# Kernel tuning notes

Hardware: AMD Instinct MI355X
Metric: run time of the kernel (lower is better)

## Reference

```python
import jax, jax.numpy as jnp
import numpy as np

N_TOKEN = 267735
CUTOFFS = [20000, 40000, 200000, 267735]
ENDS = [0] + CUTOFFS
CLUSTER_DIMS = [1024, 256, 64, 16]   # d_embed // div_val**i
CLUSTER_SIZES = [20000, 20000, 160000, 67735]
D_PROJ = 1024
T, B = 256, 4
N_CLUSTERS = 3


def setup_inputs() -> dict:
    key = jax.random.key(0)
    ks = jax.random.split(key, 16)
    inp = {}
    inp["hidden"] = jax.random.normal(ks[0], (T, B, D_PROJ), jnp.float32)
    inp["target"] = jax.random.randint(ks[1], (T, B), 0, N_TOKEN)
    for i in range(4):
        inp[f"W{i}"] = jax.random.normal(ks[2 + 3 * i], (CLUSTER_SIZES[i], CLUSTER_DIMS[i]), jnp.float32) * 0.02
        inp[f"b{i}"] = jnp.zeros((CLUSTER_SIZES[i],), jnp.float32)
        inp[f"P{i}"] = jax.random.normal(ks[3 + 3 * i], (CLUSTER_DIMS[i], D_PROJ), jnp.float32) * 0.02
    inp["cluster_weight"] = jax.random.normal(ks[14], (N_CLUSTERS, 1024), jnp.float32) * 0.02
    inp["cluster_bias"] = jnp.zeros((N_CLUSTERS,), jnp.float32)
    return inp


def _logit(x, W, b, P):
    # x: [T,B,d_proj], P: [e,d_proj], W: [n,e] -> [T,B,n]
    y = jnp.einsum('ibd,ed->ibe', x, P)
    return jnp.einsum('ibe,ne->ibn', y, W) + b


def _gather(logprob, tgt):
    # pick logprob[t, b, tgt[t,b]]
    return jnp.take_along_axis(logprob, tgt[..., None], axis=-1)[..., 0]


def reference(hidden, target, W0, b0, P0, W1, b1, P1, W2, b2, P2, W3, b3, P3,
              cluster_weight, cluster_bias):
    Ws = [W0, W1, W2, W3]
    bs = [b0, b1, b2, b3]
    Ps = [P0, P1, P2, P3]
    loss = jnp.zeros(target.shape, jnp.float32)
    head_logprob = None
    for i in range(4):
        l_idx, r_idx = ENDS[i], ENDS[i + 1]
        mask = (target >= l_idx) & (target < r_idx)
        cur_t = jnp.maximum(jnp.minimum(target, r_idx - 1) - l_idx, 0)
        if i == 0:
            Wh = jnp.concatenate([W0, cluster_weight], axis=0)
            bh = jnp.concatenate([b0, cluster_bias], axis=0)
            head_logprob = jax.nn.log_softmax(_logit(hidden, Wh, bh, P0), axis=-1)
            cur_loss = _gather(head_logprob, cur_t)
        else:
            tail_logprob = jax.nn.log_softmax(_logit(hidden, Ws[i], bs[i], Ps[i]), axis=-1)
            logprob_i = head_logprob[..., CUTOFFS[0] + i - 1, None] + tail_logprob
            cur_loss = _gather(logprob_i, cur_t)
        loss = jnp.where(mask, cur_loss, loss)
    return jnp.mean(-loss)
```

## Files before the change

kernel.cpp:

```cpp
#include <hip/hip_runtime.h>
#include <math.h>

typedef short short8 __attribute__((ext_vector_type(8)));
typedef float f32x4 __attribute__((ext_vector_type(4)));
typedef unsigned long long u64;

#define LOG2E 1.4426950408889634f

__device__ __forceinline__ unsigned short f2bf_rne(float f) {
    unsigned u = __float_as_uint(f);
    unsigned r = (u + 0x7fff + ((u >> 16) & 1)) >> 16;
    return (unsigned short)r;
}
__device__ __forceinline__ float bf2f(unsigned short h) {
    return __uint_as_float(((unsigned)h) << 16);
}
__device__ __forceinline__ void load_lds16(const void* g, void* l) {
    __builtin_amdgcn_global_load_lds((const __attribute__((address_space(1))) void*)g,
                                     (__attribute__((address_space(3))) void*)l,
                                     16, 0, 0);
}
__device__ __forceinline__ u64 pack8_fp8(const float* v, float s) {
    int lo = 0, hi = 0;
    lo = __builtin_amdgcn_cvt_pk_fp8_f32(v[0] * s, v[1] * s, lo, false);
    lo = __builtin_amdgcn_cvt_pk_fp8_f32(v[2] * s, v[3] * s, lo, true);
    hi = __builtin_amdgcn_cvt_pk_fp8_f32(v[4] * s, v[5] * s, hi, false);
    hi = __builtin_amdgcn_cvt_pk_fp8_f32(v[6] * s, v[7] * s, hi, true);
    return (u64)(unsigned)lo | ((u64)(unsigned)hi << 32);
}

__global__ void cvt_h(const float* __restrict__ in, unsigned short* __restrict__ out)
{
    const int i = blockIdx.x * 256 + threadIdx.x;
    const float4 v = *(const float4*)(in + (size_t)i * 4);
    ushort4 h;
    h.x = f2bf_rne(v.x); h.y = f2bf_rne(v.y);
    h.z = f2bf_rne(v.z); h.w = f2bf_rne(v.w);
    *(ushort4*)(out + (size_t)i * 4) = h;
}

struct ProjDesc {
    const float* B;
    unsigned short* Cbf;
    unsigned char* Cf8;
    int ldc; int nreal; int N; int Kpad; int gy_begin;
};

__global__ __launch_bounds__(256) void prepproj(
    const unsigned short* __restrict__ A,
    ProjDesc p0, ProjDesc p1, ProjDesc p2, ProjDesc p3,
    const float* __restrict__ W0, const float* __restrict__ cw,
    const float* __restrict__ W1, const float* __restrict__ W2,
    const float* __restrict__ W3,
    const float* __restrict__ b0, const float* __restrict__ cb,
    const float* __restrict__ b1, const float* __restrict__ b2,
    const float* __restrict__ b3,
    unsigned char* __restrict__ Wb0, unsigned char* __restrict__ Wb1,
    unsigned char* __restrict__ Wb2, unsigned char* __restrict__ Wb3,
    float* __restrict__ bp)
{
    __shared__ char smem[34816];

    const int tid = threadIdx.x;
    const int bx = blockIdx.x;

    if (bx >= 96) {
        const unsigned E0 = 1286144u;
        const unsigned E1 = 1613824u;
        const unsigned E2 = 2260992u;
        const unsigned E3 = 2539520u;
        const unsigned E4 = 2607520u;
        const unsigned stride = (gridDim.x - 96) * 256u;
        for (unsigned u = (bx - 96) * 256u + tid; u < E4; u += stride) {
            if (u < E3) {
                const float* src = nullptr;
                unsigned char* dstm; unsigned tile, kg2, r, tstride;
                if (u < E0) {
                    tile = u >> 13; const unsigned rem = u & 8191u;
                    kg2 = rem >> 7; r = rem & 127u;
                    const unsigned row = tile * 128u + r;
                    if (row < 20000u)      src = W0 + (size_t)row * 1024 + kg2 * 16;
                    else if (row < 20003u) src = cw + (size_t)(row - 20000u) * 1024 + kg2 * 16;
                    dstm = Wb0; tstride = 131072u;
                } else if (u < E1) {
                    const unsigned j = u - E0;
                    tile = j >> 11; const unsigned rem = j & 2047u;
                    kg2 = rem >> 7; r = rem & 127u;
                    const unsigned row = tile * 128u + r;
                    if (row < 20000u) src = W1 + (size_t)row * 256 + kg2 * 16;
                    dstm = Wb1; tstride = 32768u;
                } else if (u < E2) {
                    const unsigned j = u - E1;
                    tile = j >> 9; kg2 = (j >> 7) & 3u; r = j & 127u;
                    const unsigned row = tile * 128u + r;
                    if (row < 160000u) src = W2 + (size_t)row * 64 + kg2 * 16;
                    dstm = Wb2; tstride = 8192u;
                } else {
                    const unsigned j = u - E2;
                    tile = j >> 9; kg2 = (j >> 7) & 3u; r = j & 127u;
                    const unsigned row = tile * 128u + r;
                    if (kg2 == 0 && row < 67735u) src = W3 + (size_t)row * 16;
                    dstm = Wb3; tstride = 8192u;
                }
                float f[16];
                if (src) {
#pragma unroll
                    for (int q = 0; q < 4; ++q) {
                        const float4 v = *(const float4*)(src + q * 4);
                        f[q * 4 + 0] = v.x; f[q * 4 + 1] = v.y;
                        f[q * 4 + 2] = v.z; f[q * 4 + 3] = v.w;
                    }
                } else {
#pragma unroll
                    for (int q = 0; q < 16; ++q) f[q] = 0.f;
                }
                u64* dst = (u64*)(dstm + (size_t)tile * tstride);
                dst[(2 * kg2) * 128 + r]     = pack8_fp8(f,     16.0f);
                dst[(2 * kg2 + 1) * 128 + r] = pack8_fp8(f + 8, 16.0f);
            } else {
                const unsigned idx0 = (u - E3) * 4u;
                float e[4];
#pragma unroll
                for (int j = 0; j < 4; ++j) {
                    const unsigned idx = idx0 + j;
                    float v;
                    if (idx < 20096u) {
                        v = (idx < 20000u) ? b0[idx] * LOG2E
                          : (idx < 20003u) ? cb[idx - 20000u] * LOG2E : -1e30f;
                    } else if (idx < 40576u) {
                        const unsigned i1 = idx - 20096u;
                        v = (i1 < 20000u) ? b1[i1] * LOG2E : -1e30f;
                    } else if (idx < 202368u) {
                        const unsigned i2 = idx - 40576u;
                        v = (i2 < 160000u) ? b2[i2] * LOG2E : -1e30f;
                    } else {
                        const unsigned i3 = idx - 202368u;
                        v = (i3 < 67735u) ? b3[i3] * LOG2E : -1e30f;
                    }
                    e[j] = v;
                }
                *(float4*)(bp + idx0) = make_float4(e[0], e[1], e[2], e[3]);
            }
        }
        return;
    }

    unsigned short* As = (unsigned short*)smem;
    unsigned short* Bs = (unsigned short*)(smem + 16384);

    const int mt = bx & 7;
    const int py = bx >> 3;
    ProjDesc p = (py >= p3.gy_begin) ? p3 : (py >= p2.gy_begin) ? p2
               : (py >= p1.gy_begin) ? p1 : p0;

    const int w = tid >> 6;
    const int l = tid & 63;
    const int m0 = mt * 128;
    const int n0 = (py - p.gy_begin) * 128;
    const int wm = (w >> 1) * 64;
    const int wn = (w & 1) * 64;
    const int lane16 = l & 15;
    const int quad = l >> 4;

    const unsigned short* aptr[4];
    int ag_base[4];
#pragma unroll
    for (int i = 0; i < 4; ++i) {
        const int g = w * 256 + i * 64 + l;
        aptr[i] = A + (size_t)(m0 + (g & 127)) * 1024 + (g >> 7) * 8;
        ag_base[i] = (w * 256 + i * 64) * 8;
    }

    const int bn = tid >> 1;
    const int bhalf = tid & 1;
    int brow = n0 + bn;
    if (brow > p.N - 1) brow = p.N - 1;
    const float* brow_ptr = p.B + (size_t)brow * 1024;

    f32x4 acc[4][4] = {};

    for (int k0 = 0; k0 < 1024; k0 += 64) {
        __syncthreads();
#pragma unroll
        for (int i = 0; i < 4; ++i)
            load_lds16(aptr[i] + k0, (void*)&As[ag_base[i]]);
#pragma unroll
        for (int j = 0; j < 8; ++j) {
            const int kq = bhalf * 8 + j;
            const float4 v = *(const float4*)(brow_ptr + k0 + kq * 4);
            const unsigned px = __builtin_amdgcn_perm(__float_as_uint(v.y), __float_as_uint(v.x), 0x07060302);
            const unsigned pyv = __builtin_amdgcn_perm(__float_as_uint(v.w), __float_as_uint(v.z), 0x07060302);
            const int gran = (kq >> 1) * 128 + bn;
            *(uint2*)&Bs[gran * 8 + (kq & 1) * 4] = make_uint2(px, pyv);
        }
        __syncthreads();

#pragma unroll
        for (int kk = 0; kk < 2; ++kk) {
            const int kgb = kk * 4 + quad;
            short8 af[4], bfr[4];
#pragma unroll
            for (int mi = 0; mi < 4; ++mi)
                af[mi] = *(const short8*)&As[(kgb * 128 + wm + mi * 16 + lane16) * 8];
#pragma unroll
            for (int ni = 0; ni < 4; ++ni)
                bfr[ni] = *(const short8*)&Bs[(kgb * 128 + wn + ni * 16 + lane16) * 8];
#pragma unroll
            for (int mi = 0; mi < 4; ++mi)
#pragma unroll
                for (int ni = 0; ni < 4; ++ni)
                    acc[mi][ni] = __builtin_amdgcn_mfma_f32_16x16x32_bf16(
                        af[mi], bfr[ni], acc[mi][ni], 0, 0, 0);
        }
    }

#pragma unroll
    for (int mi = 0; mi < 4; ++mi)
#pragma unroll
        for (int ni = 0; ni < 4; ++ni) {
            const int n = n0 + wn + ni * 16 + lane16;
            if (n < p.ldc) {
#pragma unroll
                for (int r = 0; r < 4; ++r) {
                    const int m = m0 + wm + mi * 16 + quad * 4 + r;
                    const float v = (n < p.nreal) ? acc[mi][ni][r] : 0.f;
                    p.Cbf[(size_t)m * p.ldc + n] = f2bf_rne(v);
                }
            }
        }

    float* bounce = (float*)smem;
    u64* Yout = (u64*)p.Cf8 + (size_t)mt * 16 * p.Kpad;
    for (int c = 0; c < 2; ++c) {
        const int colbase = n0 + c * 64;
        if (colbase >= p.Kpad) break;
        __syncthreads();
        if ((w & 1) == c) {
#pragma unroll
            for (int mi = 0; mi < 4; ++mi)
#pragma unroll
                for (int ni = 0; ni < 4; ++ni) {
                    const int ncol = ni * 16 + lane16;
                    const bool real = (colbase + ncol) < p.nreal;
#pragma unroll
                    for (int r = 0; r < 4; ++r) {
                        const int m = wm + mi * 16 + quad * 4 + r;
                        bounce[m * 66 + ncol] = real ? acc[mi][ni][r] : 0.f;
                    }
                }
        }
        __syncthreads();
#pragma unroll
        for (int i = 0; i < 4; ++i) {
            const int g = i * 256 + tid;
            const int kgl = g >> 7;
            const int m = g & 127;
            float v[8];
#pragma unroll
            for (int j = 0; j < 8; ++j) v[j] = bounce[m * 66 + kgl * 8 + j];
            Yout[((colbase >> 3) + kgl) * 128 + m] = pack8_fp8(v, 4.0f);
        }
    }
}

struct ExpDesc {
    const unsigned char* A;
    const unsigned char* W;
    const float* bias;
    float* part;
    int Kpad; int ksl; int kmask; int gy_begin; int slab;
};

__global__ __launch_bounds__(256) void exp_gemm(ExpDesc d0, ExpDesc d1, ExpDesc d2, ExpDesc d3)
{
    __shared__ u64 As[2][1024];
    __shared__ u64 Bs[2][1024];
    __shared__ float buf[128][2];

    const int gy = blockIdx.y;
    ExpDesc d = (gy >= d3.gy_begin) ? d3 : (gy >= d2.gy_begin) ? d2
              : (gy >= d1.gy_begin) ? d1 : d0;

    const int tid = threadIdx.x;
    const int w = tid >> 6;
    const int l = tid & 63;
    const int mt = blockIdx.x;
    const int wm = (w >> 1) * 64;
    const int wn = (w & 1) * 64;
    const int lane16 = l & 15;
    const int quad = l >> 4;

    const int tiles_begin = (gy - d.gy_begin) * d.slab;
    const int T = d.slab << d.ksl;
    const int kmask = d.kmask;
    const int ksl = d.ksl;

    const size_t tstride = (size_t)128 * d.Kpad;
    const unsigned char* Abase = d.A + (size_t)mt * tstride;
    const unsigned char* Bbase = d.W + (size_t)tiles_begin * tstride;

    const int so0 = tid * 16;
    const int so1 = 4096 + tid * 16;

    load_lds16(Abase + so0, (char*)As[0] + so0);
    load_lds16(Abase + so1, (char*)As[0] + so1);
    load_lds16(Bbase + so0, (char*)Bs[0] + so0);
    load_lds16(Bbase + so1, (char*)Bs[0] + so1);

    float biasc[4], biasn[4];
#pragma unroll
    for (int ni = 0; ni < 4; ++ni)
        biasc[ni] = d.bias[tiles_begin * 128 + wn + ni * 16 + lane16];
#pragma unroll
    for (int ni = 0; ni < 4; ++ni) biasn[ni] = 0.f;

    f32x4 acc[4][4] = {};
    float rowsum[4][4] = {};
    const float c1 = LOG2E / 64.0f;

    for (int it = 0; it < T; ++it) {
        const int slot = it & 1;
        __syncthreads();

        if (it + 1 < T) {
            const int ns = slot ^ 1;
            const int kc = (it + 1) & kmask;
            if (kmask) {
                const unsigned char* ac = Abase + kc * 8192;
                load_lds16(ac + so0, (char*)As[ns] + so0);
                load_lds16(ac + so1, (char*)As[ns] + so1);
            }
            const unsigned char* bc = Bbase + (size_t)((it + 1) >> ksl) * tstride + kc * 8192;
            load_lds16(bc + so0, (char*)Bs[ns] + so0);
            load_lds16(bc + so1, (char*)Bs[ns] + so1);
            if (kc == 0) {
#pragma unroll
                for (int ni = 0; ni < 4; ++ni)
                    biasn[ni] = d.bias[(tiles_begin + ((it + 1) >> ksl)) * 128 + wn + ni * 16 + lane16];
            }
        }

        const u64* Ar = As[kmask ? slot : 0];
        const u64* Br = Bs[slot];
#pragma unroll
        for (int ks = 0; ks < 2; ++ks) {
            u64 af[4], bfr[4];
#pragma unroll
            for (int mi = 0; mi < 4; ++mi)
                af[mi] = Ar[(ks * 4 + quad) * 128 + wm + mi * 16 + lane16];
#pragma unroll
            for (int ni = 0; ni < 4; ++ni)
                bfr[ni] = Br[(ks * 4 + quad) * 128 + wn + ni * 16 + lane16];
#pragma unroll
            for (int mi = 0; mi < 4; ++mi)
#pragma unroll
                for (int ni = 0; ni < 4; ++ni)
                    acc[mi][ni] = __builtin_amdgcn_mfma_f32_16x16x32_fp8_fp8(
                        (long)af[mi], (long)bfr[ni], acc[mi][ni], 0, 0, 0);
        }

        if ((it & kmask) == kmask) {
#pragma unroll
            for (int mi = 0; mi < 4; ++mi)
#pragma unroll
                for (int r = 0; r < 4; ++r) {
                    float s = exp2f(fmaf(acc[mi][0][r], c1, biasc[0]))
                            + exp2f(fmaf(acc[mi][1][r], c1, biasc[1]))
                            + exp2f(fmaf(acc[mi][2][r], c1, biasc[2]))
                            + exp2f(fmaf(acc[mi][3][r], c1, biasc[3]));
                    rowsum[mi][r] += s;
                }
#pragma unroll
            for (int mi = 0; mi < 4; ++mi)
#pragma unroll
                for (int ni = 0; ni < 4; ++ni)
                    acc[mi][ni] = (f32x4){0.f, 0.f, 0.f, 0.f};
#pragma unroll
            for (int ni = 0; ni < 4; ++ni) biasc[ni] = biasn[ni];
        }
    }

#pragma unroll
    for (int off = 1; off < 16; off <<= 1)
#pragma unroll
        for (int mi = 0; mi < 4; ++mi)
#pragma unroll
            for (int r = 0; r < 4; ++r)
                rowsum[mi][r] += __shfl_xor(rowsum[mi][r], off, 64);

    __syncthreads();
    if (lane16 == 0) {
#pragma unroll
        for (int mi = 0; mi < 4; ++mi)
#pragma unroll
            for (int r = 0; r < 4; ++r)
                buf[wm + mi * 16 + quad * 4 + r][wn >> 6] = rowsum[mi][r];
    }
    __syncthreads();
    if (tid < 128)
        d.part[(size_t)(gy - d.gy_begin) * 1024 + mt * 128 + tid] = buf[tid][0] + buf[tid][1];
}

__global__ void redext(const float* __restrict__ p0, const float* __restrict__ p1,
                       const float* __restrict__ p2, const float* __restrict__ p3,
                       float* __restrict__ S,
                       const unsigned short* __restrict__ Y0, const unsigned short* __restrict__ Y1,
                       const unsigned short* __restrict__ Y2, const unsigned short* __restrict__ Y3,
                       const int* __restrict__ target,
                       const float* __restrict__ W0, const float* __restrict__ b0,
                       const float* __restrict__ W1, const float* __restrict__ b1,
                       const float* __restrict__ W2, const float* __restrict__ b2,
                       const float* __restrict__ W3, const float* __restrict__ b3,
                       const float* __restrict__ cw, const float* __restrict__ cb,
                       float* __restrict__ headlogit, float* __restrict__ taillogit)
{
    if (blockIdx.x < 16) {
        const int idx = blockIdx.x * 256 + threadIdx.x;
        const int c = idx >> 10, m = idx & 1023;
        const float* p = (c == 0) ? p0 : (c == 1) ? p1 : (c == 2) ? p2 : p3;
        const int G = (c == 0) ? 157 : (c == 1) ? 40 : (c == 2) ? 79 : 34;
        float s = 0.f;
        for (int y = 0; y < G; ++y) s += p[(size_t)y * 1024 + m];
        S[idx] = s;
        return;
    }
    const int token = (blockIdx.x - 16) * 4 + (threadIdx.x >> 6);
    const int lane = threadIdx.x & 63;
    const int tgt = target[token];
    const int ci = (tgt < 20000) ? 0 : (tgt < 40000) ? 1 : (tgt < 200000) ? 2 : 3;

    {
        const int h = (ci == 0) ? tgt : (20000 + ci - 1);
        const float* row;
        float bb;
        if (h < 20000) { row = W0 + (size_t)h * 1024; bb = b0[h]; }
        else           { row = cw + (size_t)(h - 20000) * 1024; bb = cb[h - 20000]; }
        const unsigned short* y = Y0 + (size_t)token * 1024;
        float s = 0.f;
        for (int k = lane; k < 1024; k += 64) s += bf2f(y[k]) * row[k];
#pragma unroll
        for (int off = 1; off < 64; off <<= 1) s += __shfl_xor(s, off, 64);
        if (lane == 0) headlogit[token] = s + bb;
    }

    float tl = 0.f;
    if (ci > 0) {
        const unsigned short* Y; const float* W; const float* b; int K, ldy, lidx;
        if (ci == 1)      { Y = Y1; W = W1; b = b1; K = 256; ldy = 256; lidx = 20000; }
        else if (ci == 2) { Y = Y2; W = W2; b = b2; K = 64;  ldy = 64;  lidx = 40000; }
        else              { Y = Y3; W = W3; b = b3; K = 16;  ldy = 64;  lidx = 200000; }
        const int r = tgt - lidx;
        const unsigned short* y = Y + (size_t)token * ldy;
        const float* row = W + (size_t)r * K;
        float s = 0.f;
        for (int k = lane; k < K; k += 64) s += bf2f(y[k]) * row[k];
#pragma unroll
        for (int off = 1; off < 64; off <<= 1) s += __shfl_xor(s, off, 64);
        tl = s + b[r];
    }
    if (lane == 0) taillogit[token] = tl;
}

__global__ void finalize_kernel(const float* __restrict__ S,
                                const int* __restrict__ target,
                                const float* __restrict__ headlogit,
                                const float* __restrict__ taillogit,
                                float* __restrict__ out)
{
    __shared__ float red[256];
    const int tid = threadIdx.x;
    float acc = 0.f;
    for (int token = tid; token < 1024; token += 256) {
        const int tgt = target[token];
        const int ci = (tgt < 20000) ? 0 : (tgt < 40000) ? 1 : (tgt < 200000) ? 2 : 3;
        float lp = headlogit[token] - logf(S[token]);
        if (ci > 0)
            lp += taillogit[token] - logf(S[ci * 1024 + token]);
        acc -= lp;
    }
    red[tid] = acc;
    __syncthreads();
    for (int s = 128; s > 0; s >>= 1) {
        if (tid < s) red[tid] += red[tid + s];
        __syncthreads();
    }
    if (tid == 0) out[0] = red[0] * (1.0f / 1024.0f);
}

extern "C" void kernel_launch(void* const* d_in, const int* in_sizes, int n_in,
                              void* d_out, int out_size, void* d_ws, size_t ws_size,
                              hipStream_t stream)
{
    const float* hidden = (const float*)d_in[0];
    const int*   target = (const int*)d_in[1];
    const float* W0 = (const float*)d_in[2];  const float* b0 = (const float*)d_in[3];  const float* P0 = (const float*)d_in[4];
    const float* W1 = (const float*)d_in[5];  const float* b1 = (const float*)d_in[6];  const float* P1 = (const float*)d_in[7];
    const float* W2 = (const float*)d_in[8];  const float* b2 = (const float*)d_in[9];  const float* P2 = (const float*)d_in[10];
    const float* W3 = (const float*)d_in[11]; const float* b3 = (const float*)d_in[12]; const float* P3 = (const float*)d_in[13];
    const float* cw = (const float*)d_in[14]; const float* cb = (const float*)d_in[15];
    float* out = (float*)d_out;

    unsigned char* ws = (unsigned char*)d_ws;
    unsigned short* h_bf = (unsigned short*)ws;
    unsigned short* Y0bf = (unsigned short*)(ws + 2097152);
    unsigned short* Y1bf = (unsigned short*)(ws + 4194304);
    unsigned short* Y2bf = (unsigned short*)(ws + 4718592);
    unsigned short* Y3bf = (unsigned short*)(ws + 4849664);
    unsigned char* Y0f8 = ws + 4980736;
    unsigned char* Y1f8 = ws + 6029312;
    unsigned char* Y2f8 = ws + 6291456;
    unsigned char* Y3f8 = ws + 6356992;
    unsigned char* Wb0 = ws + 6422528;
    unsigned char* Wb1 = ws + 27000832;
    unsigned char* Wb2 = ws + 32243712;
    unsigned char* Wb3 = ws + 42598400;
    float* bp = (float*)(ws + 47054848);

    float* part0 = (float*)ws;
    float* part1 = part0 + (size_t)157 * 1024;
    float* part2 = part1 + (size_t)40 * 1024;
    float* part3 = part2 + (size_t)79 * 1024;
    float* S = part3 + (size_t)34 * 1024;
    float* headlogit = S + 4096;
    float* taillogit = headlogit + 1024;

    cvt_h<<<1024, 256, 0, stream>>>(hidden, h_bf);

    ProjDesc pr0 = { P0, Y0bf, Y0f8, 1024, 1024, 1024, 1024, 0 };
    ProjDesc pr1 = { P1, Y1bf, Y1f8, 256,  256,  256,  256,  8 };
    ProjDesc pr2 = { P2, Y2bf, Y2f8, 64,   64,   64,   64,   10 };
    ProjDesc pr3 = { P3, Y3bf, Y3f8, 64,   16,   16,   64,   11 };
    prepproj<<<2048, 256, 0, stream>>>(h_bf, pr0, pr1, pr2, pr3,
                                       W0, cw, W1, W2, W3,
                                       b0, cb, b1, b2, b3,
                                       Wb0, Wb1, Wb2, Wb3, bp);

    ExpDesc d0 = { Y0f8, Wb0, bp,          part0, 1024, 4, 15, 0,   1 };
    ExpDesc d1 = { Y1f8, Wb1, bp + 20096,  part1, 256,  2, 3,  157, 4 };
    ExpDesc d2 = { Y2f8, Wb2, bp + 40576,  part2, 64,   0, 0,  197, 16 };
    ExpDesc d3 = { Y3f8, Wb3, bp + 202368, part3, 64,   0, 0,  276, 16 };
    exp_gemm<<<dim3(8, 310), 256, 0, stream>>>(d0, d1, d2, d3);

    redext<<<272, 256, 0, stream>>>(part0, part1, part2, part3, S,
                                    Y0bf, Y1bf, Y2bf, Y3bf, target,
                                    W0, b0, W1, b1, W2, b2, W3, b3,
                                    cw, cb, headlogit, taillogit);

    finalize_kernel<<<1, 256, 0, stream>>>(S, target, headlogit, taillogit, out);
}
```

Before: 438.6 us.

## Widen exp GEMM tile to 256 columns, fuse hidden bf16 cast into projection

The exp_gemm kernel now processes two 128-column weight tiles per block (a 128x256 output tile with 8 N-fragments per wave). This halves the grid rows and reuses each A fragment across twice as many MFMAs, at the cost of more accumulator registers and LDS. The separate cvt_h launch is removed, and the projection GEMM now reads fp32 hidden directly and converts it to bf16 while staging into LDS. The weight-repack path uses one block per fixed chunk instead of a grid-stride loop, and the slab counts, bias padding and workspace offsets are retuned to match.

```diff
diff --git a/kernel.cpp b/kernel.cpp
--- a/kernel.cpp
+++ b/kernel.cpp
@@ -29,16 +29,6 @@
     return (u64)(unsigned)lo | ((u64)(unsigned)hi << 32);
 }
 
-__global__ void cvt_h(const float* __restrict__ in, unsigned short* __restrict__ out)
-{
-    const int i = blockIdx.x * 256 + threadIdx.x;
-    const float4 v = *(const float4*)(in + (size_t)i * 4);
-    ushort4 h;
-    h.x = f2bf_rne(v.x); h.y = f2bf_rne(v.y);
-    h.z = f2bf_rne(v.z); h.w = f2bf_rne(v.w);
-    *(ushort4*)(out + (size_t)i * 4) = h;
-}
-
 struct ProjDesc {
     const float* B;
     unsigned short* Cbf;
@@ -47,7 +37,7 @@
 };
 
 __global__ __launch_bounds__(256) void prepproj(
-    const unsigned short* __restrict__ A,
+    const float* __restrict__ hidden,
     ProjDesc p0, ProjDesc p1, ProjDesc p2, ProjDesc p3,
     const float* __restrict__ W0, const float* __restrict__ cw,
     const float* __restrict__ W1, const float* __restrict__ W2,
@@ -65,79 +55,72 @@
     const int bx = blockIdx.x;
 
     if (bx >= 96) {
-        const unsigned E0 = 1286144u;
-        const unsigned E1 = 1613824u;
-        const unsigned E2 = 2260992u;
-        const unsigned E3 = 2539520u;
-        const unsigned E4 = 2607520u;
-        const unsigned stride = (gridDim.x - 96) * 256u;
-        for (unsigned u = (bx - 96) * 256u + tid; u < E4; u += stride) {
-            if (u < E3) {
-                const float* src = nullptr;
-                unsigned char* dstm; unsigned tile, kg2, r, tstride;
-                if (u < E0) {
-                    tile = u >> 13; const unsigned rem = u & 8191u;
-                    kg2 = rem >> 7; r = rem & 127u;
-                    const unsigned row = tile * 128u + r;
-                    if (row < 20000u)      src = W0 + (size_t)row * 1024 + kg2 * 16;
-                    else if (row < 20003u) src = cw + (size_t)(row - 20000u) * 1024 + kg2 * 16;
-                    dstm = Wb0; tstride = 131072u;
-                } else if (u < E1) {
-                    const unsigned j = u - E0;
-                    tile = j >> 11; const unsigned rem = j & 2047u;
-                    kg2 = rem >> 7; r = rem & 127u;
-                    const unsigned row = tile * 128u + r;
-                    if (row < 20000u) src = W1 + (size_t)row * 256 + kg2 * 16;
-                    dstm = Wb1; tstride = 32768u;
-                } else if (u < E2) {
-                    const unsigned j = u - E1;
-                    tile = j >> 9; kg2 = (j >> 7) & 3u; r = j & 127u;
-                    const unsigned row = tile * 128u + r;
-                    if (row < 160000u) src = W2 + (size_t)row * 64 + kg2 * 16;
-                    dstm = Wb2; tstride = 8192u;
-                } else {
-                    const unsigned j = u - E2;
-                    tile = j >> 9; kg2 = (j >> 7) & 3u; r = j & 127u;
-                    const unsigned row = tile * 128u + r;
-                    if (kg2 == 0 && row < 67735u) src = W3 + (size_t)row * 16;
-                    dstm = Wb3; tstride = 8192u;
+        const int v = bx - 96;
+        if (v < 9896) {
+            const float* src = nullptr;
+            u64* dst;
+            unsigned kseg, r;
+            if (v < 5056) {
+                const unsigned u = v * 256u + tid;
+                const unsigned tile = u >> 13; kseg = (u >> 7) & 63u; r = u & 127u;
+                const unsigned row = tile * 128u + r;
+                if (row < 20000u)      src = W0 + (size_t)row * 1024 + kseg * 16;
+                else if (row < 20003u) src = cw + (size_t)(row - 20000u) * 1024 + kseg * 16;
+                dst = (u64*)Wb0 + (size_t)tile * 16384;
+            } else if (v < 6336) {
+                const unsigned u = (v - 5056) * 256u + tid;
+                const unsigned tile = u >> 11; kseg = (u >> 7) & 15u; r = u & 127u;
+                const unsigned row = tile * 128u + r;
+                if (row < 20000u) src = W1 + (size_t)row * 256 + kseg * 16;
+                dst = (u64*)Wb1 + (size_t)tile * 4096;
+            } else if (v < 8836) {
+                const unsigned u = (v - 6336) * 256u + tid;
+                const unsigned tile = u >> 9; kseg = (u >> 7) & 3u; r = u & 127u;
+                src = W2 + (size_t)(tile * 128u + r) * 64 + kseg * 16;
+                dst = (u64*)Wb2 + (size_t)tile * 1024;
+            } else {
+                const unsigned u = (v - 8836) * 256u + tid;
+                const unsigned tile = u >> 9; kseg = (u >> 7) & 3u; r = u & 127u;
+                const unsigned row = tile * 128u + r;
+                if (kseg == 0 && row < 67735u) src = W3 + (size_t)row * 16;
+                dst = (u64*)Wb3 + (size_t)tile * 1024;
+            }
+            float f[16];
+            if (src) {
+#pragma unroll
+                for (int q = 0; q < 4; ++q) {
+                    const float4 x = *(const float4*)(src + q * 4);
+                    f[q * 4 + 0] = x.x; f[q * 4 + 1] = x.y;
+                    f[q * 4 + 2] = x.z; f[q * 4 + 3] = x.w;
                 }
-                float f[16];
-                if (src) {
-#pragma unroll
-                    for (int q = 0; q < 4; ++q) {
-                        const float4 v = *(const float4*)(src + q * 4);
-                        f[q * 4 + 0] = v.x; f[q * 4 + 1] = v.y;
-                        f[q * 4 + 2] = v.z; f[q * 4 + 3] = v.w;
-                    }
-                } else {
-#pragma unroll
-                    for (int q = 0; q < 16; ++q) f[q] = 0.f;
-                }
-                u64* dst = (u64*)(dstm + (size_t)tile * tstride);
-                dst[(2 * kg2) * 128 + r]     = pack8_fp8(f,     16.0f);
-                dst[(2 * kg2 + 1) * 128 + r] = pack8_fp8(f + 8, 16.0f);
             } else {
-                const unsigned idx0 = (u - E3) * 4u;
+#pragma unroll
+                for (int q = 0; q < 16; ++q) f[q] = 0.f;
+            }
+            dst[(2 * kseg) * 128 + r]     = pack8_fp8(f,     16.0f);
+            dst[(2 * kseg + 1) * 128 + r] = pack8_fp8(f + 8, 16.0f);
+        } else {
+            const unsigned u = (v - 9896) * 256u + tid;
+            if (u < 67136u) {
+                const unsigned idx0 = u * 4u;
                 float e[4];
 #pragma unroll
                 for (int j = 0; j < 4; ++j) {
                     const unsigned idx = idx0 + j;
-                    float v;
-                    if (idx < 20096u) {
-                        v = (idx < 20000u) ? b0[idx] * LOG2E
+                    float x;
+                    if (idx < 20224u) {
+                        x = (idx < 20000u) ? b0[idx] * LOG2E
                           : (idx < 20003u) ? cb[idx - 20000u] * LOG2E : -1e30f;
-                    } else if (idx < 40576u) {
-                        const unsigned i1 = idx - 20096u;
-                        v = (i1 < 20000u) ? b1[i1] * LOG2E : -1e30f;
-                    } else if (idx < 202368u) {
-                        const unsigned i2 = idx - 40576u;
-                        v = (i2 < 160000u) ? b2[i2] * LOG2E : -1e30f;
+                    } else if (idx < 40704u) {
+                        const unsigned i1 = idx - 20224u;
+                        x = (i1 < 20000u) ? b1[i1] * LOG2E : -1e30f;
+                    } else if (idx < 200704u) {
+                        x = b2[idx - 40704u] * LOG2E;
                     } else {
-                        const unsigned i3 = idx - 202368u;
-                        v = (i3 < 67735u) ? b3[i3] * LOG2E : -1e30f;
+                        const unsigned i3 = idx - 200704u;
+                        x = (i3 < 67735u) ? b3[i3] * LOG2E : -1e30f;
                     }
-                    e[j] = v;
+                    e[j] = x;
                 }
                 *(float4*)(bp + idx0) = make_float4(e[0], e[1], e[2], e[3]);
             }
@@ -162,18 +145,10 @@
     const int lane16 = l & 15;
     const int quad = l >> 4;
 
-    const unsigned short* aptr[4];
-    int ag_base[4];
-#pragma unroll
-    for (int i = 0; i < 4; ++i) {
-        const int g = w * 256 + i * 64 + l;
-        aptr[i] = A + (size_t)(m0 + (g & 127)) * 1024 + (g >> 7) * 8;
-        ag_base[i] = (w * 256 + i * 64) * 8;
-    }
-
-    const int bn = tid >> 1;
-    const int bhalf = tid & 1;
-    int brow = n0 + bn;
+    const int sn = tid >> 1;
+    const int shalf = tid & 1;
+    const float* arow_ptr = hidden + (size_t)(m0 + sn) * 1024;
+    int brow = n0 + sn;
     if (brow > p.N - 1) brow = p.N - 1;
     const float* brow_ptr = p.B + (size_t)brow * 1024;
 
@@ -182,16 +157,21 @@
     for (int k0 = 0; k0 < 1024; k0 += 64) {
         __syncthreads();
 #pragma unroll
-        for (int i = 0; i < 4; ++i)
-            load_lds16(aptr[i] + k0, (void*)&As[ag_base[i]]);
-#pragma unroll
         for (int j = 0; j < 8; ++j) {
-            const int kq = bhalf * 8 + j;
-            const float4 v = *(const float4*)(brow_ptr + k0 + kq * 4);
-            const unsigned px = __builtin_amdgcn_perm(__float_as_uint(v.y), __float_as_uint(v.x), 0x07060302);
-            const unsigned pyv = __builtin_amdgcn_perm(__float_as_uint(v.w), __float_as_uint(v.z), 0x07060302);
-            const int gran = (kq >> 1) * 128 + bn;
-            *(uint2*)&Bs[gran * 8 + (kq & 1) * 4] = make_uint2(px, pyv);
+            const int kq = shalf * 8 + j;
+            const int gran = (kq >> 1) * 128 + sn;
+            {
+                const float4 x = *(const float4*)(arow_ptr + k0 + kq * 4);
+                const unsigned px = __builtin_amdgcn_perm(__float_as_uint(x.y), __float_as_uint(x.x), 0x07060302);
+                const unsigned py2 = __builtin_amdgcn_perm(__float_as_uint(x.w), __float_as_uint(x.z), 0x07060302);
+                *(uint2*)&As[gran * 8 + (kq & 1) * 4] = make_uint2(px, py2);
+            }
+            {
+                const float4 x = *(const float4*)(brow_ptr + k0 + kq * 4);
+                const unsigned px = __builtin_amdgcn_perm(__float_as_uint(x.y), __float_as_uint(x.x), 0x07060302);
+                const unsigned py2 = __builtin_amdgcn_perm(__float_as_uint(x.w), __float_as_uint(x.z), 0x07060302);
+                *(uint2*)&Bs[gran * 8 + (kq & 1) * 4] = make_uint2(px, py2);
+            }
         }
         __syncthreads();
 
@@ -223,8 +203,8 @@
 #pragma unroll
                 for (int r = 0; r < 4; ++r) {
                     const int m = m0 + wm + mi * 16 + quad * 4 + r;
-                    const float v = (n < p.nreal) ? acc[mi][ni][r] : 0.f;
-                    p.Cbf[(size_t)m * p.ldc + n] = f2bf_rne(v);
+                    const float x = (n < p.nreal) ? acc[mi][ni][r] : 0.f;
+                    p.Cbf[(size_t)m * p.ldc + n] = f2bf_rne(x);
                 }
             }
         }
@@ -255,10 +235,10 @@
             const int g = i * 256 + tid;
             const int kgl = g >> 7;
             const int m = g & 127;
-            float v[8];
-#pragma unroll
-            for (int j = 0; j < 8; ++j) v[j] = bounce[m * 66 + kgl * 8 + j];
-            Yout[((colbase >> 3) + kgl) * 128 + m] = pack8_fp8(v, 4.0f);
+            float x[8];
+#pragma unroll
+            for (int j = 0; j < 8; ++j) x[j] = bounce[m * 66 + kgl * 8 + j];
+            Yout[((colbase >> 3) + kgl) * 128 + m] = pack8_fp8(x, 4.0f);
         }
     }
 }
@@ -274,7 +254,7 @@
 __global__ __launch_bounds__(256) void exp_gemm(ExpDesc d0, ExpDesc d1, ExpDesc d2, ExpDesc d3)
 {
     __shared__ u64 As[2][1024];
-    __shared__ u64 Bs[2][1024];
+    __shared__ u64 Bs[2][2048];
     __shared__ float buf[128][2];
 
     const int gy = blockIdx.y;
@@ -290,31 +270,38 @@
     const int lane16 = l & 15;
     const int quad = l >> 4;
 
-    const int tiles_begin = (gy - d.gy_begin) * d.slab;
+    const int dt_begin = (gy - d.gy_begin) * d.slab;
     const int T = d.slab << d.ksl;
     const int kmask = d.kmask;
     const int ksl = d.ksl;
 
     const size_t tstride = (size_t)128 * d.Kpad;
     const unsigned char* Abase = d.A + (size_t)mt * tstride;
-    const unsigned char* Bbase = d.W + (size_t)tiles_begin * tstride;
+    const unsigned char* Bbase = d.W + (size_t)(2 * dt_begin) * tstride;
 
     const int so0 = tid * 16;
-    const int so1 = 4096 + tid * 16;
+    const int so1 = so0 + 4096;
+
+    int col8[8];
+#pragma unroll
+    for (int ni = 0; ni < 8; ++ni)
+        col8[ni] = (ni >> 2) * 128 + wn + (ni & 3) * 16 + lane16;
 
     load_lds16(Abase + so0, (char*)As[0] + so0);
     load_lds16(Abase + so1, (char*)As[0] + so1);
     load_lds16(Bbase + so0, (char*)Bs[0] + so0);
     load_lds16(Bbase + so1, (char*)Bs[0] + so1);
-
-    float biasc[4], biasn[4];
-#pragma unroll
-    for (int ni = 0; ni < 4; ++ni)
-        biasc[ni] = d.bias[tiles_begin * 128 + wn + ni * 16 + lane16];
-#pragma unroll
-    for (int ni = 0; ni < 4; ++ni) biasn[ni] = 0.f;
-
-    f32x4 acc[4][4] = {};
+    load_lds16(Bbase + tstride + so0, (char*)Bs[0] + 8192 + so0);
+    load_lds16(Bbase + tstride + so1, (char*)Bs[0] + 8192 + so1);
+
+    float biasc[8], biasn[8];
+#pragma unroll
+    for (int ni = 0; ni < 8; ++ni)
+        biasc[ni] = d.bias[dt_begin * 256 + col8[ni]];
+#pragma unroll
+    for (int ni = 0; ni < 8; ++ni) biasn[ni] = 0.f;
+
+    f32x4 acc[4][8] = {};
     float rowsum[4][4] = {};
     const float c1 = LOG2E / 64.0f;
 
@@ -325,18 +312,21 @@
         if (it + 1 < T) {
             const int ns = slot ^ 1;
             const int kc = (it + 1) & kmask;
+            const int dtn = (it + 1) >> ksl;
             if (kmask) {
                 const unsigned char* ac = Abase + kc * 8192;
                 load_lds16(ac + so0, (char*)As[ns] + so0);
                 load_lds16(ac + so1, (char*)As[ns] + so1);
             }
-            const unsigned char* bc = Bbase + (size_t)((it + 1) >> ksl) * tstride + kc * 8192;
-            load_lds16(bc + so0, (char*)Bs[ns] + so0);
-            load_lds16(bc + so1, (char*)Bs[ns] + so1);
+            const unsigned char* bt = Bbase + (size_t)(2 * dtn) * tstride + kc * 8192;
+            load_lds16(bt + so0, (char*)Bs[ns] + so0);
+            load_lds16(bt + so1, (char*)Bs[ns] + so1);
+            load_lds16(bt + tstride + so0, (char*)Bs[ns] + 8192 + so0);
+            load_lds16(bt + tstride + so1, (char*)Bs[ns] + 8192 + so1);
             if (kc == 0) {
 #pragma unroll
-                for (int ni = 0; ni < 4; ++ni)
-                    biasn[ni] = d.bias[(tiles_begin + ((it + 1) >> ksl)) * 128 + wn + ni * 16 + lane16];
+                for (int ni = 0; ni < 8; ++ni)
+                    biasn[ni] = d.bias[(dt_begin + dtn) * 256 + col8[ni]];
             }
         }
 
@@ -344,17 +334,17 @@
         const u64* Br = Bs[slot];
 #pragma unroll
         for (int ks = 0; ks < 2; ++ks) {
-            u64 af[4], bfr[4];
+            u64 af[4], bfr[8];
 #pragma unroll
             for (int mi = 0; mi < 4; ++mi)
                 af[mi] = Ar[(ks * 4 + quad) * 128 + wm + mi * 16 + lane16];
 #pragma unroll
-            for (int ni = 0; ni < 4; ++ni)
-                bfr[ni] = Br[(ks * 4 + quad) * 128 + wn + ni * 16 + lane16];
-#pragma unroll
-            for (int mi = 0; mi < 4; ++mi)
-#pragma unroll
-                for (int ni = 0; ni < 4; ++ni)
+            for (int ni = 0; ni < 8; ++ni)
+                bfr[ni] = Br[(ni >> 2) * 1024 + (ks * 4 + quad) * 128 + wn + (ni & 3) * 16 + lane16];
+#pragma unroll
+            for (int mi = 0; mi < 4; ++mi)
+#pragma unroll
+                for (int ni = 0; ni < 8; ++ni)
                     acc[mi][ni] = __builtin_amdgcn_mfma_f32_16x16x32_fp8_fp8(
                         (long)af[mi], (long)bfr[ni], acc[mi][ni], 0, 0, 0);
         }
@@ -367,16 +357,20 @@
                     float s = exp2f(fmaf(acc[mi][0][r], c1, biasc[0]))
                             + exp2f(fmaf(acc[mi][1][r], c1, biasc[1]))
                             + exp2f(fmaf(acc[mi][2][r], c1, biasc[2]))
-                            + exp2f(fmaf(acc[mi][3][r], c1, biasc[3]));
+                            + exp2f(fmaf(acc[mi][3][r], c1, biasc[3]))
+                            + exp2f(fmaf(acc[mi][4][r], c1, biasc[4]))
+                            + exp2f(fmaf(acc[mi][5][r], c1, biasc[5]))
+                            + exp2f(fmaf(acc[mi][6][r], c1, biasc[6]))
+                            + exp2f(fmaf(acc[mi][7][r], c1, biasc[7]));
                     rowsum[mi][r] += s;
                 }
 #pragma unroll
             for (int mi = 0; mi < 4; ++mi)
 #pragma unroll
-                for (int ni = 0; ni < 4; ++ni)
+                for (int ni = 0; ni < 8; ++ni)
                     acc[mi][ni] = (f32x4){0.f, 0.f, 0.f, 0.f};
 #pragma unroll
-            for (int ni = 0; ni < 4; ++ni) biasc[ni] = biasn[ni];
+            for (int ni = 0; ni < 8; ++ni) biasc[ni] = biasn[ni];
         }
     }
 
@@ -418,7 +412,7 @@
         const int idx = blockIdx.x * 256 + threadIdx.x;
         const int c = idx >> 10, m = idx & 1023;
         const float* p = (c == 0) ? p0 : (c == 1) ? p1 : (c == 2) ? p2 : p3;
-        const int G = (c == 0) ? 157 : (c == 1) ? 40 : (c == 2) ? 79 : 34;
+        const int G = (c == 0) ? 79 : (c == 1) ? 20 : (c == 2) ? 25 : 53;
         float s = 0.f;
         for (int y = 0; y < G; ++y) s += p[(size_t)y * 1024 + m];
         S[idx] = s;
@@ -501,45 +495,41 @@
     float* out = (float*)d_out;
 
     unsigned char* ws = (unsigned char*)d_ws;
-    unsigned short* h_bf = (unsigned short*)ws;
-    unsigned short* Y0bf = (unsigned short*)(ws + 2097152);
-    unsigned short* Y1bf = (unsigned short*)(ws + 4194304);
-    unsigned short* Y2bf = (unsigned short*)(ws + 4718592);
-    unsigned short* Y3bf = (unsigned short*)(ws + 4849664);
-    unsigned char* Y0f8 = ws + 4980736;
-    unsigned char* Y1f8 = ws + 6029312;
-    unsigned char* Y2f8 = ws + 6291456;
-    unsigned char* Y3f8 = ws + 6356992;
-    unsigned char* Wb0 = ws + 6422528;
-    unsigned char* Wb1 = ws + 27000832;
-    unsigned char* Wb2 = ws + 32243712;
-    unsigned char* Wb3 = ws + 42598400;
-    float* bp = (float*)(ws + 47054848);
-
     float* part0 = (float*)ws;
-    float* part1 = part0 + (size_t)157 * 1024;
-    float* part2 = part1 + (size_t)40 * 1024;
-    float* part3 = part2 + (size_t)79 * 1024;
-    float* S = part3 + (size_t)34 * 1024;
+    float* part1 = part0 + (size_t)79 * 1024;
+    float* part2 = part1 + (size_t)20 * 1024;
+    float* part3 = part2 + (size_t)25 * 1024;
+    float* S = part3 + (size_t)53 * 1024;
     float* headlogit = S + 4096;
     float* taillogit = headlogit + 1024;
-
-    cvt_h<<<1024, 256, 0, stream>>>(hidden, h_bf);
+    unsigned short* Y0bf = (unsigned short*)(ws + 1048576);
+    unsigned short* Y1bf = (unsigned short*)(ws + 3145728);
+    unsigned short* Y2bf = (unsigned short*)(ws + 3670016);
+    unsigned short* Y3bf = (unsigned short*)(ws + 3801088);
+    unsigned char* Y0f8 = ws + 3932160;
+    unsigned char* Y1f8 = ws + 4980736;
+    unsigned char* Y2f8 = ws + 5242880;
+    unsigned char* Y3f8 = ws + 5308416;
+    unsigned char* Wb0 = ws + 5372928;
+    unsigned char* Wb1 = ws + 26082304;
+    unsigned char* Wb2 = ws + 31325184;
+    unsigned char* Wb3 = ws + 41565184;
+    float* bp = (float*)(ws + 45906944);
 
     ProjDesc pr0 = { P0, Y0bf, Y0f8, 1024, 1024, 1024, 1024, 0 };
     ProjDesc pr1 = { P1, Y1bf, Y1f8, 256,  256,  256,  256,  8 };
     ProjDesc pr2 = { P2, Y2bf, Y2f8, 64,   64,   64,   64,   10 };
     ProjDesc pr3 = { P3, Y3bf, Y3f8, 64,   16,   16,   64,   11 };
-    prepproj<<<2048, 256, 0, stream>>>(h_bf, pr0, pr1, pr2, pr3,
-                                       W0, cw, W1, W2, W3,
-                                       b0, cb, b1, b2, b3,
-                                       Wb0, Wb1, Wb2, Wb3, bp);
+    prepproj<<<10255, 256, 0, stream>>>(hidden, pr0, pr1, pr2, pr3,
+                                        W0, cw, W1, W2, W3,
+                                        b0, cb, b1, b2, b3,
+                                        Wb0, Wb1, Wb2, Wb3, bp);
 
     ExpDesc d0 = { Y0f8, Wb0, bp,          part0, 1024, 4, 15, 0,   1 };
-    ExpDesc d1 = { Y1f8, Wb1, bp + 20096,  part1, 256,  2, 3,  157, 4 };
-    ExpDesc d2 = { Y2f8, Wb2, bp + 40576,  part2, 64,   0, 0,  197, 16 };
-    ExpDesc d3 = { Y3f8, Wb3, bp + 202368, part3, 64,   0, 0,  276, 16 };
-    exp_gemm<<<dim3(8, 310), 256, 0, stream>>>(d0, d1, d2, d3);
+    ExpDesc d1 = { Y1f8, Wb1, bp + 20224,  part1, 256,  2, 3,  79,  4 };
+    ExpDesc d2 = { Y2f8, Wb2, bp + 40704,  part2, 64,   0, 0,  99,  25 };
+    ExpDesc d3 = { Y3f8, Wb3, bp + 200704, part3, 64,   0, 0,  124, 5 };
+    exp_gemm<<<dim3(8, 177), 256, 0, stream>>>(d0, d1, d2, d3);
 
     redext<<<272, 256, 0, stream>>>(part0, part1, part2, part3, S,
                                     Y0bf, Y1bf, Y2bf, Y3bf, target,
```

After: 459.5 us. 4.8% more time.
